# Kernel optimization log

Measured on AMD Instinct MI355X. Metric: run time of the kernel, lower is better.

Reference implementation:

```python
import jax, jax.numpy as jnp
import numpy as np
from functools import partial

N = 512
H, W = 324, 332
C = 120
NEAR, FAR, BG = 0.01, 100.0, 1.0


def setup_inputs() -> dict:
    key = jax.random.key(0)
    k1, k2, k3, k4, k5, k6 = jax.random.split(key, 6)
    # positions: small xy, depth z in [2, 8] so everything projects on screen
    xy = 0.5 * jax.random.normal(k1, (N, 2), dtype=jnp.float32)
    z = jax.random.uniform(k2, (N, 1), dtype=jnp.float32, minval=2.0, maxval=8.0)
    positions = jnp.concatenate([xy, z], axis=-1)  # [N,3]
    rotations = jax.random.normal(k3, (N, 4), dtype=jnp.float32)  # unused by the math
    # scales in [0.5, 4.5] pixels -> small footprints, early-break never triggers
    scales = jax.random.uniform(k4, (N, 3), dtype=jnp.float32) * 4.0 + 0.5
    opacities = jax.random.uniform(k5, (N,), dtype=jnp.float32)
    spectral_features = jax.random.uniform(k6, (N, C), dtype=jnp.float32)
    tone_mapping = jnp.ones((C,), dtype=jnp.float32)
    intrinsics = jnp.array([[300.0, 0.0, 166.0],
                            [0.0, 300.0, 162.0],
                            [0.0, 0.0, 1.0]], dtype=jnp.float32)
    extrinsics = jnp.eye(4, dtype=jnp.float32)
    return {"positions": positions, "rotations": rotations, "scales": scales,
            "opacities": opacities, "spectral_features": spectral_features,
            "tone_mapping": tone_mapping, "intrinsics": intrinsics,
            "extrinsics": extrinsics}


def _render(positions, scales, opacities, spectral_features, tone_mapping,
            intrinsics, extrinsics):
    # --- projection (world -> camera -> screen) ---
    ph = jnp.concatenate([positions, jnp.ones_like(positions[:, :1])], axis=-1)  # [N,4]
    cam = ph @ extrinsics.T                     # [N,4]
    cam3 = cam[:, :3]
    proj = cam3 @ intrinsics.T                  # [N,3]
    screen = proj[:, :2] / (proj[:, 2:3] + 1e-6)  # [N,2] (x, y)
    depths = cam3[:, 2]                         # [N]

    # --- frustum / screen culling mask (kept as a validity flag) ---
    valid = (depths > NEAR) & (depths < FAR)
    valid &= (screen[:, 0] > -100.0) & (screen[:, 0] < W + 100.0)
    valid &= (screen[:, 1] > -100.0) & (screen[:, 1] < H + 100.0)

    # --- 2D covariance: diag(scale_x^2, scale_y^2), regularized inverse ---
    s2 = scales[:, :2] ** 2
    cov = jnp.zeros((positions.shape[0], 2, 2), dtype=positions.dtype)
    cov = cov.at[:, 0, 0].set(s2[:, 0]).at[:, 1, 1].set(s2[:, 1])
    cov_inv = jnp.linalg.inv(cov + 1e-4 * jnp.eye(2, dtype=positions.dtype))  # [N,2,2]

    # --- depth sort (front to back) ---
    order = jnp.argsort(depths)
    screen_s = screen[order]
    depths_s = depths[order]
    cinv_s = cov_inv[order]
    op_s = opacities[order]
    valid_s = valid[order]
    spec_s = spectral_features[order]           # [N,C]

    # pixel grid: pix[h,w] = (x=w, y=h)
    X, Y = jnp.meshgrid(jnp.arange(W), jnp.arange(H))  # each [H,W]
    pix = jnp.stack([X, Y], axis=-1).astype(positions.dtype)  # [H,W,2]

    def step(A, g):
        pos, cinv, op, v = g
        done = jnp.mean(A) > 0.99  # torch early-break condition
        off = (pos[0] < -W) | (pos[0] > 2 * W) | (pos[1] < -H) | (pos[1] > 2 * H)
        skip = done | off | jnp.logical_not(v)
        diff = pix - pos                                    # [H,W,2]
        mahal = jnp.einsum('hwi,ij,hwj->hw', diff, cinv, diff)
        alpha = op * jnp.exp(-0.5 * mahal) * (1.0 - A)      # [H,W]
        alpha = jnp.where(skip, 0.0, alpha)
        return A + alpha, alpha

    A0 = jnp.zeros((H, W), dtype=positions.dtype)
    A_final, alphas = jax.lax.scan(step, A0, (screen_s, cinv_s, op_s, valid_s))  # alphas [N,H,W]

    # spectral/depth accumulation == sum_i feature_i * alpha_i (GEMM over N)
    spectral = jnp.einsum('nc,nhw->chw', spec_s, alphas)    # [C,H,W]
    depth_img = jnp.einsum('n,nhw->hw', depths_s, alphas)   # [H,W]
    spectral = spectral + BG * (1.0 - A_final)[None]
    spectral = spectral * tone_mapping[:, None, None]
    return spectral, depth_img, A_final


def reference(positions, rotations, scales, opacities, spectral_features,
              tone_mapping, intrinsics, extrinsics):
    # rotations are accepted but unused by the original math (diagonal 2D cov)
    return _render(positions, scales, opacities, spectral_features,
                   tone_mapping, intrinsics, extrinsics)
```

## Files before the change

### kernel.cpp

```cpp
#include <hip/hip_runtime.h>
#include <math.h>

#define N_G 512
#define IMG_H 324
#define IMG_W 332
#define N_C 120
#define HW (IMG_H*IMG_W)
#define CHUNK 48
#define TSX 21
#define TSY 81
#define NT (TSX*TSY)
#define NBLK (NT*4)


__global__ __launch_bounds__(256, 4) void k_render(
    const float* __restrict__ pos, const float* __restrict__ scales,
    const float* __restrict__ opac, const float* __restrict__ Km,
    const float* __restrict__ Em, const float* __restrict__ spec,
    const float* __restrict__ tm, float* __restrict__ out)
{
  __shared__ float prm[N_G*8];
  __shared__ float buf[CHUNK*64];
  __shared__ float sbuf[CHUNK*32];
  __shared__ float Tcar[64];
  __shared__ unsigned long long livem[4];
  __shared__ int wcnt[4];
  __shared__ int stopf;

  const int tid  = threadIdx.x;
  const int w    = tid >> 6;
  const int lane = tid & 63;
  const int tx = lane & 15, ty = lane >> 4;
  const unsigned long long ltm = (1ull << lane) - 1ull;

  const int t  = blockIdx.x >> 2;
  const int cq = blockIdx.x & 3;

  float psx[2], psy[2], pc00[2], pc11[2], pl2[2], pd[2];
  float bxmin[2], bxmax[2], bymin[2], bymax[2];
  {
    const float E0=Em[0],E1=Em[1],E2=Em[2],E3=Em[3],
                E4=Em[4],E5=Em[5],E6=Em[6],E7=Em[7],
                E8=Em[8],E9=Em[9],E10=Em[10],E11=Em[11];
    const float K0=Km[0],K1=Km[1],K2=Km[2],
                K3=Km[3],K4=Km[4],K5=Km[5],
                K6=Km[6],K7=Km[7],K8=Km[8];
    #pragma unroll
    for (int q = 0; q < 2; ++q) {
      const int g = w*128 + lane + q*64;
      float p0 = pos[g*3+0], p1 = pos[g*3+1], p2 = pos[g*3+2];
      float cam0 = E0*p0 + E1*p1 + E2*p2  + E3;
      float cam1 = E4*p0 + E5*p1 + E6*p2  + E7;
      float cam2 = E8*p0 + E9*p1 + E10*p2 + E11;
      float pr0 = K0*cam0 + K1*cam1 + K2*cam2;
      float pr1 = K3*cam0 + K4*cam1 + K5*cam2;
      float pr2 = K6*cam0 + K7*cam1 + K8*cam2;
      float inv = 1.0f/(pr2 + 1e-6f);
      float sx = pr0*inv, sy = pr1*inv;
      float depth = cam2;
      bool valid = (depth > 0.01f) && (depth < 100.0f)
                && (sx > -100.0f) && (sx < (float)IMG_W + 100.0f)
                && (sy > -100.0f) && (sy < (float)IMG_H + 100.0f);
      bool off = (sx < -(float)IMG_W) || (sx > 2.0f*(float)IMG_W)
              || (sy < -(float)IMG_H) || (sy > 2.0f*(float)IMG_H);
      bool skip = off || (!valid);
      float s0 = scales[g*3+0], s1 = scales[g*3+1];
      float v0 = s0*s0 + 1e-4f, v1 = s1*s1 + 1e-4f;
      const float HL2E = 0.72134752f;
      psx[q] = sx; psy[q] = sy;
      pc00[q] = HL2E/v0; pc11[q] = HL2E/v1;
      pl2[q] = __log2f(skip ? 0.0f : opac[g]);
      pd[q]  = depth;
      float rx = 6.0f*sqrtf(v0);
      float ry = 6.0f*sqrtf(v1);
      bxmin[q] = skip ?  1e9f : sx - rx;
      bxmax[q] = skip ? -1e9f : sx + rx;
      bymin[q] = skip ?  1e9f : sy - ry;
      bymax[q] = skip ? -1e9f : sy + ry;
    }
  }

  const int jx = t % TSX, ky = t / TSX;
  const int bx = 10 + ((jx & 1) ? ((jx+1)>>1) : -((jx+1)>>1));
  const int by = 40 + ((ky & 1) ? ((ky+1)>>1) : -((ky+1)>>1));

  const int x = bx*16 + tx;
  const int y = by*4 + ty;
  const bool inb = (x < IMG_W) && (y < IMG_H);
  const float px = (float)min(x, IMG_W-1);
  const float py = (float)min(y, IMG_H-1);
  const float wxmin = (float)(bx*16), wxmax = wxmin + 15.0f;
  const float wymin = (float)(by*4),  wymax = wymin + 3.0f;

  bool h0 = !(bxmin[0] > wxmax || bxmax[0] < wxmin ||
              bymin[0] > wymax || bymax[0] < wymin);
  bool h1 = !(bxmin[1] > wxmax || bxmax[1] < wxmin ||
              bymin[1] > wymax || bymax[1] < wymin);
  unsigned long long m0 = __ballot(h0), m1 = __ballot(h1);
  int c0 = __popcll(m0);
  if (lane == 0) wcnt[w] = c0 + __popcll(m1);
  if (tid == 0) stopf = 0;
  __syncthreads();
  int offw = 0;
  #pragma unroll
  for (int k = 0; k < 4; ++k) if (k < w) offw += wcnt[k];
  const int nh = wcnt[0] + wcnt[1] + wcnt[2] + wcnt[3];
  const int p0 = offw + __popcll(m0 & ltm);
  const int p1 = offw + c0 + __popcll(m1 & ltm);
  if (h0) buf[p0] = pd[0];
  if (h1) buf[p1] = pd[1];
  if (tid < 4) buf[nh + tid] = 1e30f;
  __syncthreads();

  if (h0 | h1) {
    int r0 = 0, r1 = 0;
    const float d0 = pd[0], d1 = pd[1];
    for (int j = 0; j < nh; j += 4) {
      float4 k4 = *(const float4*)&buf[j];
      if (h0) {
        r0 += (k4.x < d0 || (k4.x == d0 && j+0 < p0)) ? 1 : 0;
        r0 += (k4.y < d0 || (k4.y == d0 && j+1 < p0)) ? 1 : 0;
        r0 += (k4.z < d0 || (k4.z == d0 && j+2 < p0)) ? 1 : 0;
        r0 += (k4.w < d0 || (k4.w == d0 && j+3 < p0)) ? 1 : 0;
      }
      if (h1) {
        r1 += (k4.x < d1 || (k4.x == d1 && j+0 < p1)) ? 1 : 0;
        r1 += (k4.y < d1 || (k4.y == d1 && j+1 < p1)) ? 1 : 0;
        r1 += (k4.z < d1 || (k4.z == d1 && j+2 < p1)) ? 1 : 0;
        r1 += (k4.w < d1 || (k4.w == d1 && j+3 < p1)) ? 1 : 0;
      }
    }
    if (h0) {
      *(float4*)&prm[r0*8]   = make_float4(psx[0], psy[0], pc00[0], pc11[0]);
      *(float4*)&prm[r0*8+4] = make_float4(pl2[0], pd[0],
                                 __int_as_float((w*128 + lane)*N_C), 0.0f);
    }
    if (h1) {
      *(float4*)&prm[r1*8]   = make_float4(psx[1], psy[1], pc00[1], pc11[1]);
      *(float4*)&prm[r1*8+4] = make_float4(pl2[1], pd[1],
                                 __int_as_float((w*128 + lane + 64)*N_C), 0.0f);
    }
  }
  __syncthreads();

  float T = 1.0f, dacc = 0.0f;
  float4 acc0 = {0,0,0,0}, acc1 = {0,0,0,0};
  const int g0 = cq + 8*w;
  const bool g1ok = (g0 + 4) < 30;
  const int stc = 16*(lane >> 2) + 4*cq + (lane & 3);
  const bool stok = (lane < 32) && (stc < N_C);

  for (int cb = 0; cb < nh; cb += CHUNK) {
    if (stopf) break;
    const int nc = min(CHUNK, nh - cb);

    unsigned long long lm = 0;
    #pragma unroll 2
    for (int j = w; j < nc; j += 4) {
      float4 q0 = *(const float4*)&prm[(cb+j)*8];
      float4 q1 = *(const float4*)&prm[(cb+j)*8+4];
      float dx = px - q0.x, dy = py - q0.y;
      float m = q0.z*dx*dx + q0.w*dy*dy;
      float e = q1.x - m;
      buf[j*64 + lane] = exp2f(e);
      unsigned long long bl = __ballot(e > -24.0f);
      if (bl) {
        lm |= 1ull << j;
        int sbase = __float_as_int(q1.z);
        if (stok) sbuf[j*32 + lane] = spec[sbase + stc];
      }
    }
    if (lane == 0) livem[w] = lm;
    __syncthreads();
    const unsigned long long mask = livem[0]|livem[1]|livem[2]|livem[3];

    if (w == 0) {
      unsigned long long mb = mask;
      while (mb) {
        const int j = __builtin_ctzll(mb); mb &= mb - 1;
        float a  = buf[j*64 + lane];
        float wv = a * T;
        buf[j*64 + lane] = wv;
        if (cq == 2) dacc = fmaf(prm[(cb+j)*8+5], wv, dacc);
        T *= (1.0f - a);
      }
      unsigned long long alive = __ballot(T >= 1e-5f);
      if (lane == 0 && alive == 0ull) stopf = 1;
    }
    __syncthreads();

    unsigned long long m2 = mask;
    while (m2) {
      const int j = __builtin_ctzll(m2); m2 &= m2 - 1;
      float wv = buf[j*64 + lane];
      const float* row = &sbuf[j*32 + 8*w];
      float4 s0 = *(const float4*)(row);
      acc0.x = fmaf(wv, s0.x, acc0.x);
      acc0.y = fmaf(wv, s0.y, acc0.y);
      acc0.z = fmaf(wv, s0.z, acc0.z);
      acc0.w = fmaf(wv, s0.w, acc0.w);
      if (g1ok) {
        float4 s1 = *(const float4*)(row + 4);
        acc1.x = fmaf(wv, s1.x, acc1.x);
        acc1.y = fmaf(wv, s1.y, acc1.y);
        acc1.z = fmaf(wv, s1.z, acc1.z);
        acc1.w = fmaf(wv, s1.w, acc1.w);
      }
    }
    __syncthreads();
  }

  if (w == 0) Tcar[lane] = T;
  __syncthreads();

  if (inb) {
    const int pixi = y*IMG_W + x;
    const float bgT = Tcar[lane];
    float4 t0 = *(const float4*)&tm[4*g0];
    out[(4*g0+0)*HW + pixi] = (acc0.x + bgT)*t0.x;
    out[(4*g0+1)*HW + pixi] = (acc0.y + bgT)*t0.y;
    out[(4*g0+2)*HW + pixi] = (acc0.z + bgT)*t0.z;
    out[(4*g0+3)*HW + pixi] = (acc0.w + bgT)*t0.w;
    if (g1ok) {
      const int g1 = g0 + 4;
      float4 t1 = *(const float4*)&tm[4*g1];
      out[(4*g1+0)*HW + pixi] = (acc1.x + bgT)*t1.x;
      out[(4*g1+1)*HW + pixi] = (acc1.y + bgT)*t1.y;
      out[(4*g1+2)*HW + pixi] = (acc1.z + bgT)*t1.z;
      out[(4*g1+3)*HW + pixi] = (acc1.w + bgT)*t1.w;
    }
    if (cq == 2 && w == 0) out[N_C*HW + pixi] = dacc;
    if (cq == 3 && w == 0) out[N_C*HW + HW + pixi] = 1.0f - bgT;
  }
}

extern "C" void kernel_launch(void* const* d_in, const int* in_sizes, int n_in,
                              void* d_out, int out_size, void* d_ws, size_t ws_size,
                              hipStream_t stream) {
  const float* pos    = (const float*)d_in[0];
  const float* scales = (const float*)d_in[2];
  const float* opac   = (const float*)d_in[3];
  const float* spec   = (const float*)d_in[4];
  const float* tm     = (const float*)d_in[5];
  const float* K      = (const float*)d_in[6];
  const float* E      = (const float*)d_in[7];
  float* out = (float*)d_out;
  (void)d_ws; (void)ws_size;

  k_render<<<NBLK, 256, 0, stream>>>(pos, scales, opac, K, E, spec, tm, out);
}
```

Measured before the change: 113.7 us.

## Replace chunked shared-memory compositing with per-wave redundant alpha and direct spec loads

Removes the chunked three-phase loop (alpha compute into shared memory, single-wave transmittance scan, all-wave spectral accumulation) and its block barriers. Each wave now walks all hit gaussians itself, recomputing alpha and transmittance redundantly, and loads spectral features straight from global memory (cached) instead of staging them in shared memory. Shared memory shrinks, so launch bounds are raised to allow six blocks per CU. The trade is four-fold redundant exp and transmittance work, plus global loads inside the serial loop, in exchange for no barriers and higher occupancy.

Measured after the change: 122.9 us. +8.1%, slower.

```diff
diff --git a/kernel.cpp b/kernel.cpp
--- a/kernel.cpp
+++ b/kernel.cpp
@@ -6,26 +6,21 @@
 #define IMG_W 332
 #define N_C 120
 #define HW (IMG_H*IMG_W)
-#define CHUNK 48
 #define TSX 21
 #define TSY 81
 #define NT (TSX*TSY)
 #define NBLK (NT*4)
 
 
-__global__ __launch_bounds__(256, 4) void k_render(
+__global__ __launch_bounds__(256, 6) void k_render(
     const float* __restrict__ pos, const float* __restrict__ scales,
     const float* __restrict__ opac, const float* __restrict__ Km,
     const float* __restrict__ Em, const float* __restrict__ spec,
     const float* __restrict__ tm, float* __restrict__ out)
 {
   __shared__ float prm[N_G*8];
-  __shared__ float buf[CHUNK*64];
-  __shared__ float sbuf[CHUNK*32];
-  __shared__ float Tcar[64];
-  __shared__ unsigned long long livem[4];
+  __shared__ float key[N_G+4];
   __shared__ int wcnt[4];
-  __shared__ int stopf;
 
   const int tid  = threadIdx.x;
   const int w    = tid >> 6;
@@ -99,7 +94,6 @@
   unsigned long long m0 = __ballot(h0), m1 = __ballot(h1);
   int c0 = __popcll(m0);
   if (lane == 0) wcnt[w] = c0 + __popcll(m1);
-  if (tid == 0) stopf = 0;
   __syncthreads();
   int offw = 0;
   #pragma unroll
@@ -107,16 +101,16 @@
   const int nh = wcnt[0] + wcnt[1] + wcnt[2] + wcnt[3];
   const int p0 = offw + __popcll(m0 & ltm);
   const int p1 = offw + c0 + __popcll(m1 & ltm);
-  if (h0) buf[p0] = pd[0];
-  if (h1) buf[p1] = pd[1];
-  if (tid < 4) buf[nh + tid] = 1e30f;
+  if (h0) key[p0] = pd[0];
+  if (h1) key[p1] = pd[1];
+  if (tid < 4) key[nh + tid] = 1e30f;
   __syncthreads();
 
   if (h0 | h1) {
     int r0 = 0, r1 = 0;
     const float d0 = pd[0], d1 = pd[1];
     for (int j = 0; j < nh; j += 4) {
-      float4 k4 = *(const float4*)&buf[j];
+      float4 k4 = *(const float4*)&key[j];
       if (h0) {
         r0 += (k4.x < d0 || (k4.x == d0 && j+0 < p0)) ? 1 : 0;
         r0 += (k4.y < d0 || (k4.y == d0 && j+1 < p0)) ? 1 : 0;
@@ -147,75 +141,39 @@
   float4 acc0 = {0,0,0,0}, acc1 = {0,0,0,0};
   const int g0 = cq + 8*w;
   const bool g1ok = (g0 + 4) < 30;
-  const int stc = 16*(lane >> 2) + 4*cq + (lane & 3);
-  const bool stok = (lane < 32) && (stc < N_C);
-
-  for (int cb = 0; cb < nh; cb += CHUNK) {
-    if (stopf) break;
-    const int nc = min(CHUNK, nh - cb);
-
-    unsigned long long lm = 0;
-    #pragma unroll 2
-    for (int j = w; j < nc; j += 4) {
-      float4 q0 = *(const float4*)&prm[(cb+j)*8];
-      float4 q1 = *(const float4*)&prm[(cb+j)*8+4];
-      float dx = px - q0.x, dy = py - q0.y;
-      float m = q0.z*dx*dx + q0.w*dy*dy;
-      float e = q1.x - m;
-      buf[j*64 + lane] = exp2f(e);
-      unsigned long long bl = __ballot(e > -24.0f);
-      if (bl) {
-        lm |= 1ull << j;
-        int sbase = __float_as_int(q1.z);
-        if (stok) sbuf[j*32 + lane] = spec[sbase + stc];
-      }
-    }
-    if (lane == 0) livem[w] = lm;
-    __syncthreads();
-    const unsigned long long mask = livem[0]|livem[1]|livem[2]|livem[3];
-
-    if (w == 0) {
-      unsigned long long mb = mask;
-      while (mb) {
-        const int j = __builtin_ctzll(mb); mb &= mb - 1;
-        float a  = buf[j*64 + lane];
-        float wv = a * T;
-        buf[j*64 + lane] = wv;
-        if (cq == 2) dacc = fmaf(prm[(cb+j)*8+5], wv, dacc);
-        T *= (1.0f - a);
-      }
-      unsigned long long alive = __ballot(T >= 1e-5f);
-      if (lane == 0 && alive == 0ull) stopf = 1;
-    }
-    __syncthreads();
-
-    unsigned long long m2 = mask;
-    while (m2) {
-      const int j = __builtin_ctzll(m2); m2 &= m2 - 1;
-      float wv = buf[j*64 + lane];
-      const float* row = &sbuf[j*32 + 8*w];
-      float4 s0 = *(const float4*)(row);
+  const float* specg0 = spec + 4*g0;
+
+  #pragma unroll 2
+  for (int j = 0; j < nh; ++j) {
+    float4 q0 = *(const float4*)&prm[j*8];
+    float4 q1 = *(const float4*)&prm[j*8+4];
+    float dx = px - q0.x, dy = py - q0.y;
+    float e = q1.x - (q0.z*dx*dx + q0.w*dy*dy);
+    if (__ballot(e > -30.0f)) {
+      float a  = exp2f(e);
+      float wv = a * T;
+      T *= (1.0f - a);
+      if (cq == 2) dacc = fmaf(q1.y, wv, dacc);
+      const int sbase = __float_as_int(q1.z);
+      float4 s0 = *(const float4*)(specg0 + sbase);
       acc0.x = fmaf(wv, s0.x, acc0.x);
       acc0.y = fmaf(wv, s0.y, acc0.y);
       acc0.z = fmaf(wv, s0.z, acc0.z);
       acc0.w = fmaf(wv, s0.w, acc0.w);
       if (g1ok) {
-        float4 s1 = *(const float4*)(row + 4);
+        float4 s1 = *(const float4*)(specg0 + sbase + 16);
         acc1.x = fmaf(wv, s1.x, acc1.x);
         acc1.y = fmaf(wv, s1.y, acc1.y);
         acc1.z = fmaf(wv, s1.z, acc1.z);
         acc1.w = fmaf(wv, s1.w, acc1.w);
       }
-    }
-    __syncthreads();
-  }
-
-  if (w == 0) Tcar[lane] = T;
-  __syncthreads();
+      if (!__ballot(T >= 1e-5f)) break;
+    }
+  }
 
   if (inb) {
     const int pixi = y*IMG_W + x;
-    const float bgT = Tcar[lane];
+    const float bgT = T;
     float4 t0 = *(const float4*)&tm[4*g0];
     out[(4*g0+0)*HW + pixi] = (acc0.x + bgT)*t0.x;
     out[(4*g0+1)*HW + pixi] = (acc0.y + bgT)*t0.y;
@@ -230,7 +188,7 @@
       out[(4*g1+3)*HW + pixi] = (acc1.w + bgT)*t1.w;
     }
     if (cq == 2 && w == 0) out[N_C*HW + pixi] = dacc;
-    if (cq == 3 && w == 0) out[N_C*HW + HW + pixi] = 1.0f - bgT;
+    if (cq == 3 && w == 0) out[N_C*HW + HW + pixi] = 1.0f - T;
   }
 }
 
```
